# Optimization experiments

Measured on AMD Instinct MI355X. Metric: run time of the kernel, lower is better.

Reference implementation:

```python
import jax, jax.numpy as jnp
import numpy as np

HIDDEN = 2048
NUM_HEADS = 32
NUM_KV_HEADS = 8
GROUP = NUM_HEADS // NUM_KV_HEADS  # 4
HEAD_DIM = HIDDEN // NUM_HEADS     # 64
SEQ = 2048


def setup_inputs() -> dict:
    key = jax.random.key(0)
    ks = jax.random.split(key, 5)
    s = HIDDEN ** -0.5
    x = jax.random.normal(ks[0], (SEQ, HIDDEN), jnp.float32)
    q_proj = jax.random.normal(ks[1], (HIDDEN, HIDDEN), jnp.float32) * s
    k_proj = jax.random.normal(ks[2], (HIDDEN, HIDDEN // GROUP), jnp.float32) * s
    v_proj = jax.random.normal(ks[3], (HIDDEN, HIDDEN // GROUP), jnp.float32) * s
    o_proj = jax.random.normal(ks[4], (HIDDEN, HIDDEN), jnp.float32) * s
    # inv_freq = 1/rsqrt(10000**(i/d)) = sqrt(10000**(i/d)) per the original module
    inv_freq = jnp.sqrt(10000.0 ** (jnp.arange(0, HEAD_DIM, 2) / HEAD_DIM)).astype(jnp.float32)
    return {"x": x, "q_proj": q_proj, "k_proj": k_proj, "v_proj": v_proj,
            "o_proj": o_proj, "inv_freq": inv_freq}


def _rope(x, inv_freq):
    # x: [S, ..., HEAD_DIM]; rotation per the original (nonstandard) formula.
    orig_dtype = x.dtype
    x = x.astype(jnp.float32)
    seq = jnp.arange(x.shape[0])
    angles = seq[:, None] * jax.lax.stop_gradient(inv_freq)[None, :]  # [S, HEAD_DIM//2]
    bshape = (x.shape[0],) + (1,) * (x.ndim - 2) + (HEAD_DIM // 2,)
    sins = jnp.sin(angles).reshape(bshape)
    coss = jnp.cos(angles).reshape(bshape)
    half, odd = jnp.split(x, 2, axis=-1)
    out = jnp.concatenate([half * coss + odd * sins, half * sins - odd * coss], axis=-1)
    return out.astype(orig_dtype)


def reference(x, q_proj, k_proj, v_proj, o_proj, inv_freq):
    S = x.shape[0]
    q = (x @ q_proj).reshape(S, NUM_KV_HEADS, GROUP, HEAD_DIM)
    k = (x @ k_proj).reshape(S, NUM_KV_HEADS, HEAD_DIM)
    v = (x @ v_proj).reshape(S, NUM_KV_HEADS, HEAD_DIM)
    q = _rope(q, inv_freq)
    k = _rope(k, inv_freq)
    # scores: [a=S, b=S, h=kv_heads, g=group]
    scores = jnp.einsum('ahgd,bhd->abhg', q, k) / (HEAD_DIM ** 0.5)
    mask = jnp.tril(jnp.ones((S, S), dtype=jnp.bool_))[:, :, None, None]
    scores = jnp.where(mask, scores, -jnp.inf)
    attn = jax.nn.softmax(scores, axis=1)  # softmax over b (axis=-3)
    o = jnp.einsum('abhg,bhd->ahgd', attn, v).reshape(S, HIDDEN)
    return o @ o_proj
```

## Files before the change

kernel.cpp:

```cpp
#include <hip/hip_runtime.h>


typedef __bf16 bf16_t;
typedef __bf16 bf16x4 __attribute__((ext_vector_type(4)));
typedef __bf16 bf16x8 __attribute__((ext_vector_type(8)));
typedef float  f32x4  __attribute__((ext_vector_type(4)));
typedef short  s16x4  __attribute__((ext_vector_type(4)));

#define S_LEN   2048
#define HID     2048
#define NKV     8
#define NH      32
#define DHEAD   64
#define KVW     (NKV * DHEAD)

__device__ __align__(16) bf16_t g_xb [S_LEN * HID];
__device__ __align__(16) bf16_t g_wTq[HID * HID];
__device__ __align__(16) bf16_t g_wTk[KVW * HID];
__device__ __align__(16) bf16_t g_wTv[KVW * HID];
__device__ __align__(16) bf16_t g_wTo[HID * HID];
__device__ __align__(16) bf16_t g_q [S_LEN * HID];
__device__ __align__(16) bf16_t g_k [S_LEN * KVW];
__device__ __align__(16) bf16_t g_vT[KVW * S_LEN];
__device__ __align__(16) bf16_t g_om[S_LEN * HID];
__device__ float g_ropeC[S_LEN * 32];
__device__ float g_ropeS[S_LEN * 32];
__device__ __align__(16) float g_po[4u * S_LEN * HID];
__device__ float g_pl[4u * S_LEN * NH];

static __device__ inline s16x4 bc4(bf16x4 v) { s16x4 r; __builtin_memcpy(&r, &v, 8); return r; }

__device__ __forceinline__ void gll16(void* lds, const void* g) {
    __builtin_amdgcn_global_load_lds(
        (const __attribute__((address_space(1))) void*)g,
        (__attribute__((address_space(3))) void*)lds,
        16, 0, 0);
}

__global__ __launch_bounds__(256)
void prep_kernel(const float* __restrict__ x,
                 const float* __restrict__ qw, const float* __restrict__ kw,
                 const float* __restrict__ vw, const float* __restrict__ ow,
                 const void* __restrict__ invf_raw) {
    __shared__ bf16_t tile[64][65];
    int b = blockIdx.x, t = threadIdx.x;

    if (b < 256) {
        int idx = b * 256 + t;
        int s = idx >> 5, j = idx & 31;
        float f;
        if (*(const unsigned*)invf_raw == 0x3F800000u) {
            f = ((const float*)invf_raw)[j];
        } else {
            unsigned u = ((unsigned)((const unsigned short*)invf_raw)[j]) << 16;
            __builtin_memcpy(&f, &u, 4);
        }
        double a = (double)s * (double)f;
        g_ropeC[idx] = (float)cos(a);
        g_ropeS[idx] = (float)sin(a);
        return;
    }
    if (b < 4352) {
        int idx = (b - 256) * 256 + t;
        float4 v = reinterpret_cast<const float4*>(x)[idx];
        bf16x4 o;
        o[0] = (bf16_t)v.x; o[1] = (bf16_t)v.y; o[2] = (bf16_t)v.z; o[3] = (bf16_t)v.w;
        *reinterpret_cast<bf16x4*>(&g_xb[(size_t)idx * 4]) = o;
        return;
    }
    const float* in; bf16_t* outp; int R, C, tb;
    if (b < 5376)      { in = qw; outp = g_wTq; R = HID; C = HID; tb = b - 4352; }
    else if (b < 5632) { in = kw; outp = g_wTk; R = HID; C = KVW; tb = b - 5376; }
    else if (b < 5888) { in = vw; outp = g_wTv; R = HID; C = KVW; tb = b - 5632; }
    else               { in = ow; outp = g_wTo; R = HID; C = HID; tb = b - 5888; }
    int xt = C >> 6;
    int c0 = (tb % xt) * 64, r0 = (tb / xt) * 64;
    int tx = t & 63, ty = t >> 6;
    #pragma unroll
    for (int r = ty; r < 64; r += 4)
        tile[r][tx] = (bf16_t)in[(size_t)(r0 + r) * C + c0 + tx];
    __syncthreads();
    #pragma unroll
    for (int r = ty; r < 64; r += 4)
        outp[(size_t)(c0 + r) * R + r0 + tx] = tile[tx][r];
}

__global__ __launch_bounds__(256)
void gemm_fused_kernel(float* __restrict__ Cf, int which) {
    __shared__ __align__(16) bf16_t As[2][128 * 64];
    __shared__ __align__(16) bf16_t Bs[2][64 * 64];

    int t    = threadIdx.x;
    int lane = t & 63, wid = t >> 6;
    int quad = lane >> 4, l15 = lane & 15;

    int ntn  = (which == 1) ? 32 : 48;
    int nwg  = ntn * 16;
    int orig = blockIdx.x;
    int qq   = nwg >> 3;
    int wg   = (orig & 7) * qq + (orig >> 3);
    int my   = wg / ntn, nx = wg - my * ntn;
    int m0   = my * 128;

    const bf16_t* A; const bf16_t* Bt; int n0;
    if (which == 1)      { A = g_om; Bt = g_wTo; n0 = nx * 64; }
    else {
        A = g_xb;
        if (nx < 32)      { Bt = g_wTq; n0 = nx * 64; }
        else if (nx < 40) { Bt = g_wTk; n0 = (nx - 32) * 64; }
        else              { Bt = g_wTv; n0 = (nx - 40) * 64; }
    }

    int crow = lane >> 3;
    int gseg = (lane & 7) ^ crow;
    int so   = l15 & 7;
    int wm   = wid * 32;

    f32x4 acc[2][4];
    #pragma unroll
    for (int im = 0; im < 2; ++im)
        #pragma unroll
        for (int in = 0; in < 4; ++in)
            #pragma unroll
            for (int r = 0; r < 4; ++r) acc[im][in][r] = 0.f;

    auto stage = [&](int buf, int kt) {
        #pragma unroll
        for (int c = 0; c < 4; ++c)
            gll16(&As[buf][(wid * 4 + c) * 512],
                  A  + (size_t)(m0 + (wid * 4 + c) * 8 + crow) * HID + kt + gseg * 8);
        #pragma unroll
        for (int c = 0; c < 2; ++c)
            gll16(&Bs[buf][(wid * 2 + c) * 512],
                  Bt + (size_t)(n0 + (wid * 2 + c) * 8 + crow) * HID + kt + gseg * 8);
    };

    stage(0, 0);

    for (int it = 0; it < 32; ++it) {
        int cur = it & 1;
        if (it + 1 < 32) {
            stage(cur ^ 1, (it + 1) * 64);
            asm volatile("s_waitcnt vmcnt(6)" ::: "memory");
        } else {
            asm volatile("s_waitcnt vmcnt(0)" ::: "memory");
        }
        asm volatile("s_barrier" ::: "memory");

        #pragma unroll
        for (int kh = 0; kh < 2; ++kh) {
            bf16x8 af[2], bfv[4];
            #pragma unroll
            for (int i = 0; i < 2; ++i)
                af[i]  = *reinterpret_cast<const bf16x8*>(
                    &As[cur][(wm + i * 16 + l15) * 64 + (((kh * 4 + quad) ^ so) * 8)]);
            #pragma unroll
            for (int i = 0; i < 4; ++i)
                bfv[i] = *reinterpret_cast<const bf16x8*>(
                    &Bs[cur][(i * 16 + l15) * 64 + (((kh * 4 + quad) ^ so) * 8)]);
            #pragma unroll
            for (int im = 0; im < 2; ++im)
                #pragma unroll
                for (int in = 0; in < 4; ++in)
                    acc[im][in] = __builtin_amdgcn_mfma_f32_16x16x32_bf16(
                        af[im], bfv[in], acc[im][in], 0, 0, 0);
        }

        asm volatile("s_barrier" ::: "memory");
    }

    if (which == 1) {
        #pragma unroll
        for (int im = 0; im < 2; ++im) {
            int rowb = m0 + wm + im * 16 + quad * 4;
            #pragma unroll
            for (int in = 0; in < 4; ++in) {
                int col = n0 + in * 16 + l15;
                #pragma unroll
                for (int r = 0; r < 4; ++r)
                    Cf[(size_t)(rowb + r) * HID + col] = acc[im][in][r];
            }
        }
    } else if (nx < 40) {
        bf16_t* Cb; int N, colbase;
        if (nx < 32) { Cb = g_q; N = HID; colbase = nx * 64; }
        else         { Cb = g_k; N = KVW; colbase = (nx - 32) * 64; }
        #pragma unroll
        for (int im = 0; im < 2; ++im) {
            #pragma unroll
            for (int r = 0; r < 4; ++r) {
                int row = m0 + wm + im * 16 + quad * 4 + r;
                #pragma unroll
                for (int in = 0; in < 2; ++in) {
                    int d = in * 16 + l15;
                    float a  = acc[im][in][r];
                    float bb = acc[im][in + 2][r];
                    float cc = g_ropeC[row * 32 + d];
                    float ss = g_ropeS[row * 32 + d];
                    Cb[(size_t)row * N + colbase + d]      = (bf16_t)(a * cc + bb * ss);
                    Cb[(size_t)row * N + colbase + 32 + d] = (bf16_t)(a * ss - bb * cc);
                }
            }
        }
    } else {
        #pragma unroll
        for (int im = 0; im < 2; ++im) {
            int rowb = m0 + wm + im * 16 + quad * 4;
            #pragma unroll
            for (int in = 0; in < 4; ++in) {
                int col = (nx - 40) * 64 + in * 16 + l15;
                #pragma unroll
                for (int r = 0; r < 4; ++r)
                    g_vT[(size_t)col * S_LEN + (rowb + r)] = (bf16_t)acc[im][in][r];
            }
        }
    }
}

__global__ __launch_bounds__(256)
void flash_part_kernel() {
    __shared__ __align__(16) bf16_t Ks[2][64 * 64];
    __shared__ __align__(16) bf16_t Vs[2][64 * 64];

    int t    = threadIdx.x;
    int lane = t & 63, wid = t >> 6;
    int quad = lane >> 4, l15 = lane & 15;
    int bx   = blockIdx.x;
    int hk   = bx & 7;
    int qb32 = (bx >> 3) & 63;
    int chunk = bx >> 9;
    int nkt  = (qb32 >> 1) + 1;
    int kt0  = chunk * 8;
    if (kt0 >= nkt) return;
    int kt1  = min(kt0 + 8, nkt);
    int nt   = kt1 - kt0;

    int head = hk * 4 + wid;
    int q0   = qb32 * 32;

    int crow = lane >> 3;
    int gseg = (lane & 7) ^ crow;
    int so   = l15 & 7;

    bf16x8 aq[2][2];
    #pragma unroll
    for (int mq = 0; mq < 2; ++mq) {
        const bf16_t* qp = g_q + (size_t)(q0 + mq * 16 + l15) * HID + head * 64 + quad * 8;
        aq[mq][0] = *reinterpret_cast<const bf16x8*>(qp);
        aq[mq][1] = *reinterpret_cast<const bf16x8*>(qp + 32);
        #pragma unroll
        for (int j = 0; j < 8; ++j) {
            aq[mq][0][j] = (bf16_t)((float)aq[mq][0][j] * 0.125f);
            aq[mq][1][j] = (bf16_t)((float)aq[mq][1][j] * 0.125f);
        }
    }

    bf16x4 ones4;
    #pragma unroll
    for (int j = 0; j < 4; ++j) ones4[j] = (bf16_t)1.0f;
    s16x4 ones_s = bc4(ones4);

    f32x4 oacc[2][4], liacc[2];
    #pragma unroll
    for (int mq = 0; mq < 2; ++mq) {
        #pragma unroll
        for (int r = 0; r < 4; ++r) liacc[mq][r] = 0.f;
        #pragma unroll
        for (int dt = 0; dt < 4; ++dt)
            #pragma unroll
            for (int r = 0; r < 4; ++r) oacc[mq][dt][r] = 0.f;
    }

    int qcol[2] = { q0 + l15, q0 + 16 + l15 };

    auto stageKV = [&](int buf, int k0) {
        #pragma unroll
        for (int c = 0; c < 2; ++c) {
            int ch = wid * 2 + c;
            gll16(&Ks[buf][ch * 512],
                  g_k  + (size_t)(k0 + ch * 8 + crow) * KVW + hk * 64 + gseg * 8);
            gll16(&Vs[buf][ch * 512],
                  g_vT + (size_t)(hk * 64 + ch * 8 + crow) * S_LEN + k0 + gseg * 8);
        }
    };

    stageKV(0, kt0 * 64);

    for (int i = 0; i < nt; ++i) {
        int cur = i & 1;
        int k0  = (kt0 + i) * 64;
        if (i + 1 < nt) {
            stageKV(cur ^ 1, (kt0 + i + 1) * 64);
            asm volatile("s_waitcnt vmcnt(4)" ::: "memory");
        } else {
            asm volatile("s_waitcnt vmcnt(0)" ::: "memory");
        }
        asm volatile("s_barrier" ::: "memory");

        bf16x8 ak[4][2];
        #pragma unroll
        for (int mk = 0; mk < 4; ++mk) {
            int row = mk * 16 + l15;
            ak[mk][0] = *reinterpret_cast<const bf16x8*>(&Ks[cur][row * 64 + ((quad ^ so) * 8)]);
            ak[mk][1] = *reinterpret_cast<const bf16x8*>(&Ks[cur][row * 64 + (((4 + quad) ^ so) * 8)]);
        }

        f32x4 sacc[4][2];
        #pragma unroll
        for (int mk = 0; mk < 4; ++mk)
            #pragma unroll
            for (int mq = 0; mq < 2; ++mq) {
                f32x4 s;
                #pragma unroll
                for (int r = 0; r < 4; ++r) s[r] = 0.f;
                s = __builtin_amdgcn_mfma_f32_16x16x32_bf16(ak[mk][0], aq[mq][0], s, 0, 0, 0);
                s = __builtin_amdgcn_mfma_f32_16x16x32_bf16(ak[mk][1], aq[mq][1], s, 0, 0, 0);
                sacc[mk][mq] = s;
            }

        s16x4 pas[4][2];
        #pragma unroll
        for (int mk = 0; mk < 4; ++mk)
            #pragma unroll
            for (int mq = 0; mq < 2; ++mq) {
                bf16x4 pa;
                #pragma unroll
                for (int r = 0; r < 4; ++r) {
                    int kk = k0 + mk * 16 + quad * 4 + r;
                    pa[r] = (bf16_t)((kk <= qcol[mq]) ? __expf(sacc[mk][mq][r] - 16.0f) : 0.0f);
                }
                pas[mk][mq] = bc4(pa);
            }

        #pragma unroll
        for (int mk = 0; mk < 4; ++mk) {
            #pragma unroll
            for (int dt = 0; dt < 4; ++dt) {
                int rv = dt * 16 + l15;
                int vb = rv * 64 + (((mk * 2 + (quad >> 1)) ^ so) * 8) + (quad & 1) * 4;
                bf16x4 bv = *reinterpret_cast<const bf16x4*>(&Vs[cur][vb]);
                s16x4 bvs = bc4(bv);
                #pragma unroll
                for (int mq = 0; mq < 2; ++mq)
                    oacc[mq][dt] = __builtin_amdgcn_mfma_f32_16x16x16bf16_1k(pas[mk][mq], bvs, oacc[mq][dt], 0, 0, 0);
            }
            #pragma unroll
            for (int mq = 0; mq < 2; ++mq)
                liacc[mq] = __builtin_amdgcn_mfma_f32_16x16x16bf16_1k(pas[mk][mq], ones_s, liacc[mq], 0, 0, 0);
        }

        asm volatile("s_barrier" ::: "memory");
    }

    float* po = g_po + (size_t)chunk * S_LEN * HID;
    #pragma unroll
    for (int mq = 0; mq < 2; ++mq)
        #pragma unroll
        for (int r = 0; r < 4; ++r) {
            int row = q0 + mq * 16 + quad * 4 + r;
            #pragma unroll
            for (int dt = 0; dt < 4; ++dt)
                po[(size_t)row * HID + head * 64 + dt * 16 + l15] = oacc[mq][dt][r];
            if (l15 == 0)
                g_pl[((size_t)chunk * S_LEN + row) * NH + head] = liacc[mq][r];
        }
}

__global__ __launch_bounds__(256)
void flash_combine_kernel() {
    int t = blockIdx.x * 256 + threadIdx.x;
    int row  = t >> 9;
    int col4 = (t & 511) * 4;
    int head = col4 >> 6;
    int nkt  = ((row >> 5) >> 1) + 1;
    int nc   = (nkt + 7) >> 3;

    float4 s = make_float4(0.f, 0.f, 0.f, 0.f);
    float l = 0.f;
    for (int c = 0; c < nc; ++c) {
        const float4 v = *reinterpret_cast<const float4*>(
            g_po + ((size_t)c * S_LEN + row) * HID + col4);
        s.x += v.x; s.y += v.y; s.z += v.z; s.w += v.w;
        l += g_pl[((size_t)c * S_LEN + row) * NH + head];
    }
    float inv = 1.0f / l;
    bf16x4 o;
    o[0] = (bf16_t)(s.x * inv); o[1] = (bf16_t)(s.y * inv);
    o[2] = (bf16_t)(s.z * inv); o[3] = (bf16_t)(s.w * inv);
    *reinterpret_cast<bf16x4*>(&g_om[(size_t)row * HID + col4]) = o;
}

extern "C" void kernel_launch(void* const* d_in, const int* in_sizes, int n_in,
                              void* d_out, int out_size, void* d_ws, size_t ws_size,
                              hipStream_t stream) {
    const float* x    = (const float*)d_in[0];
    const float* qpW  = (const float*)d_in[1];
    const float* kpW  = (const float*)d_in[2];
    const float* vpW  = (const float*)d_in[3];
    const float* opW  = (const float*)d_in[4];
    const void*  invf = d_in[5];
    float* out = (float*)d_out;

    prep_kernel<<<6912, 256, 0, stream>>>(x, qpW, kpW, vpW, opW, invf);
    gemm_fused_kernel<<<768, 256, 0, stream>>>(nullptr, 0);
    flash_part_kernel<<<2048, 256, 0, stream>>>();
    flash_combine_kernel<<<4096, 256, 0, stream>>>();
    gemm_fused_kernel<<<512, 256, 0, stream>>>(out, 1);
}
```

Baseline: 246.4 us.

## Halve GEMM M-tile to 64x64 with 2x2 wave layout and MFMA priority hints

The GEMM kernel's output tile shrinks from 128x64 to 64x64, with waves arranged 2x2. The grid doubles for both the QKV projection and the output projection, which gives more workgroups and more parallelism on the GPU's many CUs. The price is less data reuse per tile, since each tile now runs 4 MFMAs per k-half instead of 8. s_setprio hints are also placed around the MFMA blocks in both the GEMM and the flash kernel. Separately, the RoPE angle is now computed in float before the double cos/sin, so it matches the reference's float32 angle rounding.

```diff
diff --git a/kernel.cpp b/kernel.cpp
--- a/kernel.cpp
+++ b/kernel.cpp
@@ -55,7 +55,8 @@
             unsigned u = ((unsigned)((const unsigned short*)invf_raw)[j]) << 16;
             __builtin_memcpy(&f, &u, 4);
         }
-        double a = (double)s * (double)f;
+        float a32 = (float)s * f;
+        double a = (double)a32;
         g_ropeC[idx] = (float)cos(a);
         g_ropeS[idx] = (float)sin(a);
         return;
@@ -87,7 +88,7 @@
 
 __global__ __launch_bounds__(256)
 void gemm_fused_kernel(float* __restrict__ Cf, int which) {
-    __shared__ __align__(16) bf16_t As[2][128 * 64];
+    __shared__ __align__(16) bf16_t As[2][64 * 64];
     __shared__ __align__(16) bf16_t Bs[2][64 * 64];
 
     int t    = threadIdx.x;
@@ -95,12 +96,12 @@
     int quad = lane >> 4, l15 = lane & 15;
 
     int ntn  = (which == 1) ? 32 : 48;
-    int nwg  = ntn * 16;
+    int nwg  = ntn * 32;
     int orig = blockIdx.x;
     int qq   = nwg >> 3;
     int wg   = (orig & 7) * qq + (orig >> 3);
     int my   = wg / ntn, nx = wg - my * ntn;
-    int m0   = my * 128;
+    int m0   = my * 64;
 
     const bf16_t* A; const bf16_t* Bt; int n0;
     if (which == 1)      { A = g_om; Bt = g_wTo; n0 = nx * 64; }
@@ -114,25 +115,26 @@
     int crow = lane >> 3;
     int gseg = (lane & 7) ^ crow;
     int so   = l15 & 7;
-    int wm   = wid * 32;
-
-    f32x4 acc[2][4];
+    int wr   = (wid >> 1) * 32;
+    int wc   = (wid & 1) * 16;
+
+    f32x4 acc[2][2];
     #pragma unroll
     for (int im = 0; im < 2; ++im)
         #pragma unroll
-        for (int in = 0; in < 4; ++in)
+        for (int in = 0; in < 2; ++in)
             #pragma unroll
             for (int r = 0; r < 4; ++r) acc[im][in][r] = 0.f;
 
     auto stage = [&](int buf, int kt) {
         #pragma unroll
-        for (int c = 0; c < 4; ++c)
-            gll16(&As[buf][(wid * 4 + c) * 512],
-                  A  + (size_t)(m0 + (wid * 4 + c) * 8 + crow) * HID + kt + gseg * 8);
-        #pragma unroll
-        for (int c = 0; c < 2; ++c)
-            gll16(&Bs[buf][(wid * 2 + c) * 512],
-                  Bt + (size_t)(n0 + (wid * 2 + c) * 8 + crow) * HID + kt + gseg * 8);
+        for (int c = 0; c < 2; ++c) {
+            int ch = wid * 2 + c;
+            gll16(&As[buf][ch * 512],
+                  A  + (size_t)(m0 + ch * 8 + crow) * HID + kt + gseg * 8);
+            gll16(&Bs[buf][ch * 512],
+                  Bt + (size_t)(n0 + ch * 8 + crow) * HID + kt + gseg * 8);
+        }
     };
 
     stage(0, 0);
@@ -141,7 +143,7 @@
         int cur = it & 1;
         if (it + 1 < 32) {
             stage(cur ^ 1, (it + 1) * 64);
-            asm volatile("s_waitcnt vmcnt(6)" ::: "memory");
+            asm volatile("s_waitcnt vmcnt(4)" ::: "memory");
         } else {
             asm volatile("s_waitcnt vmcnt(0)" ::: "memory");
         }
@@ -149,21 +151,23 @@
 
         #pragma unroll
         for (int kh = 0; kh < 2; ++kh) {
-            bf16x8 af[2], bfv[4];
-            #pragma unroll
-            for (int i = 0; i < 2; ++i)
-                af[i]  = *reinterpret_cast<const bf16x8*>(
-                    &As[cur][(wm + i * 16 + l15) * 64 + (((kh * 4 + quad) ^ so) * 8)]);
-            #pragma unroll
-            for (int i = 0; i < 4; ++i)
-                bfv[i] = *reinterpret_cast<const bf16x8*>(
-                    &Bs[cur][(i * 16 + l15) * 64 + (((kh * 4 + quad) ^ so) * 8)]);
+            bf16x8 af[2], bfv[2];
             #pragma unroll
             for (int im = 0; im < 2; ++im)
-                #pragma unroll
-                for (int in = 0; in < 4; ++in)
+                af[im]  = *reinterpret_cast<const bf16x8*>(
+                    &As[cur][(wr + im * 16 + l15) * 64 + (((kh * 4 + quad) ^ so) * 8)]);
+            #pragma unroll
+            for (int in = 0; in < 2; ++in)
+                bfv[in] = *reinterpret_cast<const bf16x8*>(
+                    &Bs[cur][(wc + in * 32 + l15) * 64 + (((kh * 4 + quad) ^ so) * 8)]);
+            __builtin_amdgcn_s_setprio(1);
+            #pragma unroll
+            for (int im = 0; im < 2; ++im)
+                #pragma unroll
+                for (int in = 0; in < 2; ++in)
                     acc[im][in] = __builtin_amdgcn_mfma_f32_16x16x32_bf16(
                         af[im], bfv[in], acc[im][in], 0, 0, 0);
+            __builtin_amdgcn_s_setprio(0);
         }
 
         asm volatile("s_barrier" ::: "memory");
@@ -172,10 +176,10 @@
     if (which == 1) {
         #pragma unroll
         for (int im = 0; im < 2; ++im) {
-            int rowb = m0 + wm + im * 16 + quad * 4;
-            #pragma unroll
-            for (int in = 0; in < 4; ++in) {
-                int col = n0 + in * 16 + l15;
+            int rowb = m0 + wr + im * 16 + quad * 4;
+            #pragma unroll
+            for (int in = 0; in < 2; ++in) {
+                int col = n0 + wc + in * 32 + l15;
                 #pragma unroll
                 for (int r = 0; r < 4; ++r)
                     Cf[(size_t)(rowb + r) * HID + col] = acc[im][in][r];
@@ -189,26 +193,23 @@
         for (int im = 0; im < 2; ++im) {
             #pragma unroll
             for (int r = 0; r < 4; ++r) {
-                int row = m0 + wm + im * 16 + quad * 4 + r;
-                #pragma unroll
-                for (int in = 0; in < 2; ++in) {
-                    int d = in * 16 + l15;
-                    float a  = acc[im][in][r];
-                    float bb = acc[im][in + 2][r];
-                    float cc = g_ropeC[row * 32 + d];
-                    float ss = g_ropeS[row * 32 + d];
-                    Cb[(size_t)row * N + colbase + d]      = (bf16_t)(a * cc + bb * ss);
-                    Cb[(size_t)row * N + colbase + 32 + d] = (bf16_t)(a * ss - bb * cc);
-                }
+                int row = m0 + wr + im * 16 + quad * 4 + r;
+                int d   = wc + l15;
+                float a  = acc[im][0][r];
+                float bb = acc[im][1][r];
+                float cc = g_ropeC[row * 32 + d];
+                float ss = g_ropeS[row * 32 + d];
+                Cb[(size_t)row * N + colbase + d]      = (bf16_t)(a * cc + bb * ss);
+                Cb[(size_t)row * N + colbase + 32 + d] = (bf16_t)(a * ss - bb * cc);
             }
         }
     } else {
         #pragma unroll
         for (int im = 0; im < 2; ++im) {
-            int rowb = m0 + wm + im * 16 + quad * 4;
-            #pragma unroll
-            for (int in = 0; in < 4; ++in) {
-                int col = (nx - 40) * 64 + in * 16 + l15;
+            int rowb = m0 + wr + im * 16 + quad * 4;
+            #pragma unroll
+            for (int in = 0; in < 2; ++in) {
+                int col = (nx - 40) * 64 + wc + in * 32 + l15;
                 #pragma unroll
                 for (int r = 0; r < 4; ++r)
                     g_vT[(size_t)col * S_LEN + (rowb + r)] = (bf16_t)acc[im][in][r];
@@ -306,6 +307,7 @@
         }
 
         f32x4 sacc[4][2];
+        __builtin_amdgcn_s_setprio(1);
         #pragma unroll
         for (int mk = 0; mk < 4; ++mk)
             #pragma unroll
@@ -317,6 +319,7 @@
                 s = __builtin_amdgcn_mfma_f32_16x16x32_bf16(ak[mk][1], aq[mq][1], s, 0, 0, 0);
                 sacc[mk][mq] = s;
             }
+        __builtin_amdgcn_s_setprio(0);
 
         s16x4 pas[4][2];
         #pragma unroll
@@ -332,6 +335,7 @@
                 pas[mk][mq] = bc4(pa);
             }
 
+        __builtin_amdgcn_s_setprio(1);
         #pragma unroll
         for (int mk = 0; mk < 4; ++mk) {
             #pragma unroll
@@ -348,6 +352,7 @@
             for (int mq = 0; mq < 2; ++mq)
                 liacc[mq] = __builtin_amdgcn_mfma_f32_16x16x16bf16_1k(pas[mk][mq], ones_s, liacc[mq], 0, 0, 0);
         }
+        __builtin_amdgcn_s_setprio(0);
 
         asm volatile("s_barrier" ::: "memory");
     }
@@ -402,8 +407,8 @@
     float* out = (float*)d_out;
 
     prep_kernel<<<6912, 256, 0, stream>>>(x, qpW, kpW, vpW, opW, invf);
-    gemm_fused_kernel<<<768, 256, 0, stream>>>(nullptr, 0);
+    gemm_fused_kernel<<<1536, 256, 0, stream>>>(nullptr, 0);
     flash_part_kernel<<<2048, 256, 0, stream>>>();
     flash_combine_kernel<<<4096, 256, 0, stream>>>();
-    gemm_fused_kernel<<<512, 256, 0, stream>>>(out, 1);
-}
+    gemm_fused_kernel<<<1024, 256, 0, stream>>>(out, 1);
+}
```

New measurement: 270.2 us. +9.7%, slower.

## Triple-buffer LDS in GEMM and flash kernels, vectorize weight transpose loads

Applied to the files above, without the earlier changes.

The GEMM and flash attention kernels move from two LDS buffers to three, prefetching two tiles ahead. Each loop now has one barrier instead of two, so loads overlap compute more and sync overhead drops. The prep transpose reads float4 vectors instead of scalars, and the RoPE angle is computed in float before the double trig. The cost is more LDS per block, which may lower occupancy, and the vmcnt counts must match the deeper pipeline.

```diff
diff --git a/kernel.cpp b/kernel.cpp
--- a/kernel.cpp
+++ b/kernel.cpp
@@ -55,7 +55,8 @@
             unsigned u = ((unsigned)((const unsigned short*)invf_raw)[j]) << 16;
             __builtin_memcpy(&f, &u, 4);
         }
-        double a = (double)s * (double)f;
+        float a32 = (float)s * f;
+        double a = (double)a32;
         g_ropeC[idx] = (float)cos(a);
         g_ropeS[idx] = (float)sin(a);
         return;
@@ -75,20 +76,27 @@
     else               { in = ow; outp = g_wTo; R = HID; C = HID; tb = b - 5888; }
     int xt = C >> 6;
     int c0 = (tb % xt) * 64, r0 = (tb / xt) * 64;
-    int tx = t & 63, ty = t >> 6;
-    #pragma unroll
-    for (int r = ty; r < 64; r += 4)
-        tile[r][tx] = (bf16_t)in[(size_t)(r0 + r) * C + c0 + tx];
+    int tx4 = t & 15, ty = t >> 4;
+    #pragma unroll
+    for (int r = ty; r < 64; r += 16) {
+        float4 v = *reinterpret_cast<const float4*>(
+            &in[(size_t)(r0 + r) * C + c0 + tx4 * 4]);
+        tile[r][tx4 * 4 + 0] = (bf16_t)v.x;
+        tile[r][tx4 * 4 + 1] = (bf16_t)v.y;
+        tile[r][tx4 * 4 + 2] = (bf16_t)v.z;
+        tile[r][tx4 * 4 + 3] = (bf16_t)v.w;
+    }
     __syncthreads();
-    #pragma unroll
-    for (int r = ty; r < 64; r += 4)
-        outp[(size_t)(c0 + r) * R + r0 + tx] = tile[tx][r];
+    int wx = t & 63, wy = t >> 6;
+    #pragma unroll
+    for (int r = wy; r < 64; r += 4)
+        outp[(size_t)(c0 + r) * R + r0 + wx] = tile[wx][r];
 }
 
 __global__ __launch_bounds__(256)
 void gemm_fused_kernel(float* __restrict__ Cf, int which) {
-    __shared__ __align__(16) bf16_t As[2][128 * 64];
-    __shared__ __align__(16) bf16_t Bs[2][64 * 64];
+    __shared__ __align__(16) bf16_t As[3][128 * 64];
+    __shared__ __align__(16) bf16_t Bs[3][64 * 64];
 
     int t    = threadIdx.x;
     int lane = t & 63, wid = t >> 6;
@@ -136,16 +144,15 @@
     };
 
     stage(0, 0);
+    stage(1, 64);
 
     for (int it = 0; it < 32; ++it) {
-        int cur = it & 1;
-        if (it + 1 < 32) {
-            stage(cur ^ 1, (it + 1) * 64);
-            asm volatile("s_waitcnt vmcnt(6)" ::: "memory");
-        } else {
-            asm volatile("s_waitcnt vmcnt(0)" ::: "memory");
-        }
+        int cur = it % 3;
+        if (it + 1 < 32) { asm volatile("s_waitcnt vmcnt(6)" ::: "memory"); }
+        else             { asm volatile("s_waitcnt vmcnt(0)" ::: "memory"); }
         asm volatile("s_barrier" ::: "memory");
+        if (it + 2 < 32)
+            stage((it + 2) % 3, (it + 2) * 64);
 
         #pragma unroll
         for (int kh = 0; kh < 2; ++kh) {
@@ -165,8 +172,6 @@
                     acc[im][in] = __builtin_amdgcn_mfma_f32_16x16x32_bf16(
                         af[im], bfv[in], acc[im][in], 0, 0, 0);
         }
-
-        asm volatile("s_barrier" ::: "memory");
     }
 
     if (which == 1) {
@@ -219,8 +224,8 @@
 
 __global__ __launch_bounds__(256)
 void flash_part_kernel() {
-    __shared__ __align__(16) bf16_t Ks[2][64 * 64];
-    __shared__ __align__(16) bf16_t Vs[2][64 * 64];
+    __shared__ __align__(16) bf16_t Ks[3][64 * 64];
+    __shared__ __align__(16) bf16_t Vs[3][64 * 64];
 
     int t    = threadIdx.x;
     int lane = t & 63, wid = t >> 6;
@@ -285,17 +290,16 @@
     };
 
     stageKV(0, kt0 * 64);
+    if (nt > 1) stageKV(1, (kt0 + 1) * 64);
 
     for (int i = 0; i < nt; ++i) {
-        int cur = i & 1;
+        int cur = i % 3;
         int k0  = (kt0 + i) * 64;
-        if (i + 1 < nt) {
-            stageKV(cur ^ 1, (kt0 + i + 1) * 64);
-            asm volatile("s_waitcnt vmcnt(4)" ::: "memory");
-        } else {
-            asm volatile("s_waitcnt vmcnt(0)" ::: "memory");
-        }
+        if (i + 1 < nt) { asm volatile("s_waitcnt vmcnt(4)" ::: "memory"); }
+        else            { asm volatile("s_waitcnt vmcnt(0)" ::: "memory"); }
         asm volatile("s_barrier" ::: "memory");
+        if (i + 2 < nt)
+            stageKV((i + 2) % 3, (kt0 + i + 2) * 64);
 
         bf16x8 ak[4][2];
         #pragma unroll
@@ -348,8 +352,6 @@
             for (int mq = 0; mq < 2; ++mq)
                 liacc[mq] = __builtin_amdgcn_mfma_f32_16x16x16bf16_1k(pas[mk][mq], ones_s, liacc[mq], 0, 0, 0);
         }
-
-        asm volatile("s_barrier" ::: "memory");
     }
 
     float* po = g_po + (size_t)chunk * S_LEN * HID;
```

New measurement: 268.8 us. 1.09x slower.

## Split flash KV range across two wave groups in-block, drop global combine kernel

Applied to the files above, without the earlier changes.

Rewrites the attention kernel to use 512-thread blocks in which two 4-wave groups handle alternating KV tiles for the same 32 query rows. The two partial results are merged through shared memory instead of through global fp32 partial buffers and a separate combine kernel. Query blocks are ordered so long and short causal rows are interleaved for load balance. It also vectorises the fp32 loads in the weight transpose and computes the rope angle in fp32. The cost is twice the LDS per block, fewer blocks in flight, and the full causal range for a row now runs inside a single block.

```diff
diff --git a/kernel.cpp b/kernel.cpp
--- a/kernel.cpp
+++ b/kernel.cpp
@@ -25,8 +25,6 @@
 __device__ __align__(16) bf16_t g_om[S_LEN * HID];
 __device__ float g_ropeC[S_LEN * 32];
 __device__ float g_ropeS[S_LEN * 32];
-__device__ __align__(16) float g_po[4u * S_LEN * HID];
-__device__ float g_pl[4u * S_LEN * NH];
 
 static __device__ inline s16x4 bc4(bf16x4 v) { s16x4 r; __builtin_memcpy(&r, &v, 8); return r; }
 
@@ -55,7 +53,8 @@
             unsigned u = ((unsigned)((const unsigned short*)invf_raw)[j]) << 16;
             __builtin_memcpy(&f, &u, 4);
         }
-        double a = (double)s * (double)f;
+        float a32 = (float)s * f;
+        double a = (double)a32;
         g_ropeC[idx] = (float)cos(a);
         g_ropeS[idx] = (float)sin(a);
         return;
@@ -75,14 +74,21 @@
     else               { in = ow; outp = g_wTo; R = HID; C = HID; tb = b - 5888; }
     int xt = C >> 6;
     int c0 = (tb % xt) * 64, r0 = (tb / xt) * 64;
-    int tx = t & 63, ty = t >> 6;
-    #pragma unroll
-    for (int r = ty; r < 64; r += 4)
-        tile[r][tx] = (bf16_t)in[(size_t)(r0 + r) * C + c0 + tx];
+    int tx4 = t & 15, ty = t >> 4;
+    #pragma unroll
+    for (int r = ty; r < 64; r += 16) {
+        float4 v = *reinterpret_cast<const float4*>(
+            &in[(size_t)(r0 + r) * C + c0 + tx4 * 4]);
+        tile[r][tx4 * 4 + 0] = (bf16_t)v.x;
+        tile[r][tx4 * 4 + 1] = (bf16_t)v.y;
+        tile[r][tx4 * 4 + 2] = (bf16_t)v.z;
+        tile[r][tx4 * 4 + 3] = (bf16_t)v.w;
+    }
     __syncthreads();
-    #pragma unroll
-    for (int r = ty; r < 64; r += 4)
-        outp[(size_t)(c0 + r) * R + r0 + tx] = tile[tx][r];
+    int wx = t & 63, wy = t >> 6;
+    #pragma unroll
+    for (int r = wy; r < 64; r += 4)
+        outp[(size_t)(c0 + r) * R + r0 + wx] = tile[wx][r];
 }
 
 __global__ __launch_bounds__(256)
@@ -217,25 +223,23 @@
     }
 }
 
-__global__ __launch_bounds__(256)
+__global__ __launch_bounds__(512)
 void flash_part_kernel() {
-    __shared__ __align__(16) bf16_t Ks[2][64 * 64];
-    __shared__ __align__(16) bf16_t Vs[2][64 * 64];
+    __shared__ __align__(16) bf16_t SM[2][2][2][64 * 64];
 
     int t    = threadIdx.x;
     int lane = t & 63, wid = t >> 6;
+    int g    = wid >> 2;
+    int wh   = wid & 3;
     int quad = lane >> 4, l15 = lane & 15;
     int bx   = blockIdx.x;
     int hk   = bx & 7;
-    int qb32 = (bx >> 3) & 63;
-    int chunk = bx >> 9;
+    int slot = bx >> 3;
+    int qb32 = (slot & 1) ? (slot >> 1) : (63 - (slot >> 1));
     int nkt  = (qb32 >> 1) + 1;
-    int kt0  = chunk * 8;
-    if (kt0 >= nkt) return;
-    int kt1  = min(kt0 + 8, nkt);
-    int nt   = kt1 - kt0;
-
-    int head = hk * 4 + wid;
+    int ng   = (nkt + 1) >> 1;
+
+    int head = hk * 4 + wh;
     int q0   = qb32 * 32;
 
     int crow = lane >> 3;
@@ -276,118 +280,119 @@
     auto stageKV = [&](int buf, int k0) {
         #pragma unroll
         for (int c = 0; c < 2; ++c) {
-            int ch = wid * 2 + c;
-            gll16(&Ks[buf][ch * 512],
+            int ch = wh * 2 + c;
+            gll16(&SM[g][0][buf][ch * 512],
                   g_k  + (size_t)(k0 + ch * 8 + crow) * KVW + hk * 64 + gseg * 8);
-            gll16(&Vs[buf][ch * 512],
+            gll16(&SM[g][1][buf][ch * 512],
                   g_vT + (size_t)(hk * 64 + ch * 8 + crow) * S_LEN + k0 + gseg * 8);
         }
     };
 
-    stageKV(0, kt0 * 64);
-
-    for (int i = 0; i < nt; ++i) {
-        int cur = i & 1;
-        int k0  = (kt0 + i) * 64;
-        if (i + 1 < nt) {
-            stageKV(cur ^ 1, (kt0 + i + 1) * 64);
+    if (g < nkt) stageKV(0, g * 64);
+
+    for (int i = 0; i < ng; ++i) {
+        int cur  = i & 1;
+        int kt   = 2 * i + g;
+        bool live = (kt < nkt);
+        int ktn  = kt + 2;
+        bool stage_next = (i + 1 < ng) && (ktn < nkt);
+        if (stage_next) {
+            stageKV(cur ^ 1, ktn * 64);
             asm volatile("s_waitcnt vmcnt(4)" ::: "memory");
         } else {
             asm volatile("s_waitcnt vmcnt(0)" ::: "memory");
         }
         asm volatile("s_barrier" ::: "memory");
 
-        bf16x8 ak[4][2];
-        #pragma unroll
-        for (int mk = 0; mk < 4; ++mk) {
-            int row = mk * 16 + l15;
-            ak[mk][0] = *reinterpret_cast<const bf16x8*>(&Ks[cur][row * 64 + ((quad ^ so) * 8)]);
-            ak[mk][1] = *reinterpret_cast<const bf16x8*>(&Ks[cur][row * 64 + (((4 + quad) ^ so) * 8)]);
-        }
-
-        f32x4 sacc[4][2];
-        #pragma unroll
-        for (int mk = 0; mk < 4; ++mk)
-            #pragma unroll
-            for (int mq = 0; mq < 2; ++mq) {
-                f32x4 s;
-                #pragma unroll
-                for (int r = 0; r < 4; ++r) s[r] = 0.f;
-                s = __builtin_amdgcn_mfma_f32_16x16x32_bf16(ak[mk][0], aq[mq][0], s, 0, 0, 0);
-                s = __builtin_amdgcn_mfma_f32_16x16x32_bf16(ak[mk][1], aq[mq][1], s, 0, 0, 0);
-                sacc[mk][mq] = s;
-            }
-
-        s16x4 pas[4][2];
-        #pragma unroll
-        for (int mk = 0; mk < 4; ++mk)
-            #pragma unroll
-            for (int mq = 0; mq < 2; ++mq) {
-                bf16x4 pa;
-                #pragma unroll
-                for (int r = 0; r < 4; ++r) {
-                    int kk = k0 + mk * 16 + quad * 4 + r;
-                    pa[r] = (bf16_t)((kk <= qcol[mq]) ? __expf(sacc[mk][mq][r] - 16.0f) : 0.0f);
+        if (live) {
+            int k0 = kt * 64;
+            bf16x8 ak[4][2];
+            #pragma unroll
+            for (int mk = 0; mk < 4; ++mk) {
+                int row = mk * 16 + l15;
+                ak[mk][0] = *reinterpret_cast<const bf16x8*>(&SM[g][0][cur][row * 64 + ((quad ^ so) * 8)]);
+                ak[mk][1] = *reinterpret_cast<const bf16x8*>(&SM[g][0][cur][row * 64 + (((4 + quad) ^ so) * 8)]);
+            }
+
+            f32x4 sacc[4][2];
+            #pragma unroll
+            for (int mk = 0; mk < 4; ++mk)
+                #pragma unroll
+                for (int mq = 0; mq < 2; ++mq) {
+                    f32x4 s;
+                    #pragma unroll
+                    for (int r = 0; r < 4; ++r) s[r] = 0.f;
+                    s = __builtin_amdgcn_mfma_f32_16x16x32_bf16(ak[mk][0], aq[mq][0], s, 0, 0, 0);
+                    s = __builtin_amdgcn_mfma_f32_16x16x32_bf16(ak[mk][1], aq[mq][1], s, 0, 0, 0);
+                    sacc[mk][mq] = s;
                 }
-                pas[mk][mq] = bc4(pa);
-            }
-
-        #pragma unroll
-        for (int mk = 0; mk < 4; ++mk) {
-            #pragma unroll
-            for (int dt = 0; dt < 4; ++dt) {
-                int rv = dt * 16 + l15;
-                int vb = rv * 64 + (((mk * 2 + (quad >> 1)) ^ so) * 8) + (quad & 1) * 4;
-                bf16x4 bv = *reinterpret_cast<const bf16x4*>(&Vs[cur][vb]);
-                s16x4 bvs = bc4(bv);
+
+            s16x4 pas[4][2];
+            #pragma unroll
+            for (int mk = 0; mk < 4; ++mk)
+                #pragma unroll
+                for (int mq = 0; mq < 2; ++mq) {
+                    bf16x4 pa;
+                    #pragma unroll
+                    for (int r = 0; r < 4; ++r) {
+                        int kk = k0 + mk * 16 + quad * 4 + r;
+                        pa[r] = (bf16_t)((kk <= qcol[mq]) ? __expf(sacc[mk][mq][r] - 16.0f) : 0.0f);
+                    }
+                    pas[mk][mq] = bc4(pa);
+                }
+
+            #pragma unroll
+            for (int mk = 0; mk < 4; ++mk) {
+                #pragma unroll
+                for (int dt = 0; dt < 4; ++dt) {
+                    int rv = dt * 16 + l15;
+                    int vb = rv * 64 + (((mk * 2 + (quad >> 1)) ^ so) * 8) + (quad & 1) * 4;
+                    bf16x4 bv = *reinterpret_cast<const bf16x4*>(&SM[g][1][cur][vb]);
+                    s16x4 bvs = bc4(bv);
+                    #pragma unroll
+                    for (int mq = 0; mq < 2; ++mq)
+                        oacc[mq][dt] = __builtin_amdgcn_mfma_f32_16x16x16bf16_1k(pas[mk][mq], bvs, oacc[mq][dt], 0, 0, 0);
+                }
                 #pragma unroll
                 for (int mq = 0; mq < 2; ++mq)
-                    oacc[mq][dt] = __builtin_amdgcn_mfma_f32_16x16x16bf16_1k(pas[mk][mq], bvs, oacc[mq][dt], 0, 0, 0);
-            }
-            #pragma unroll
-            for (int mq = 0; mq < 2; ++mq)
-                liacc[mq] = __builtin_amdgcn_mfma_f32_16x16x16bf16_1k(pas[mk][mq], ones_s, liacc[mq], 0, 0, 0);
+                    liacc[mq] = __builtin_amdgcn_mfma_f32_16x16x16bf16_1k(pas[mk][mq], ones_s, liacc[mq], 0, 0, 0);
+            }
         }
 
         asm volatile("s_barrier" ::: "memory");
     }
 
-    float* po = g_po + (size_t)chunk * S_LEN * HID;
-    #pragma unroll
-    for (int mq = 0; mq < 2; ++mq)
-        #pragma unroll
-        for (int r = 0; r < 4; ++r) {
-            int row = q0 + mq * 16 + quad * 4 + r;
-            #pragma unroll
-            for (int dt = 0; dt < 4; ++dt)
-                po[(size_t)row * HID + head * 64 + dt * 16 + l15] = oacc[mq][dt][r];
-            if (l15 == 0)
-                g_pl[((size_t)chunk * S_LEN + row) * NH + head] = liacc[mq][r];
-        }
-}
-
-__global__ __launch_bounds__(256)
-void flash_combine_kernel() {
-    int t = blockIdx.x * 256 + threadIdx.x;
-    int row  = t >> 9;
-    int col4 = (t & 511) * 4;
-    int head = col4 >> 6;
-    int nkt  = ((row >> 5) >> 1) + 1;
-    int nc   = (nkt + 7) >> 3;
-
-    float4 s = make_float4(0.f, 0.f, 0.f, 0.f);
-    float l = 0.f;
-    for (int c = 0; c < nc; ++c) {
-        const float4 v = *reinterpret_cast<const float4*>(
-            g_po + ((size_t)c * S_LEN + row) * HID + col4);
-        s.x += v.x; s.y += v.y; s.z += v.z; s.w += v.w;
-        l += g_pl[((size_t)c * S_LEN + row) * NH + head];
-    }
-    float inv = 1.0f / l;
-    bf16x4 o;
-    o[0] = (bf16_t)(s.x * inv); o[1] = (bf16_t)(s.y * inv);
-    o[2] = (bf16_t)(s.z * inv); o[3] = (bf16_t)(s.w * inv);
-    *reinterpret_cast<bf16x4*>(&g_om[(size_t)row * HID + col4]) = o;
+    float* pO = reinterpret_cast<float*>(&SM[1][0][0][0]);
+    float* pl = reinterpret_cast<float*>(&SM[0][0][0][0]);
+    if (g == 1) {
+        #pragma unroll
+        for (int mq = 0; mq < 2; ++mq)
+            #pragma unroll
+            for (int r = 0; r < 4; ++r) {
+                int row = mq * 16 + quad * 4 + r;
+                #pragma unroll
+                for (int dt = 0; dt < 4; ++dt)
+                    pO[(wh * 32 + row) * 64 + dt * 16 + l15] = oacc[mq][dt][r];
+                if (l15 == 0) pl[wh * 32 + row] = liacc[mq][r];
+            }
+    }
+    asm volatile("s_waitcnt lgkmcnt(0)" ::: "memory");
+    asm volatile("s_barrier" ::: "memory");
+    if (g == 0) {
+        #pragma unroll
+        for (int mq = 0; mq < 2; ++mq)
+            #pragma unroll
+            for (int r = 0; r < 4; ++r) {
+                int row = mq * 16 + quad * 4 + r;
+                float l = liacc[mq][r] + pl[wh * 32 + row];
+                float inv = 1.0f / l;
+                #pragma unroll
+                for (int dt = 0; dt < 4; ++dt) {
+                    float o = oacc[mq][dt][r] + pO[(wh * 32 + row) * 64 + dt * 16 + l15];
+                    g_om[(size_t)(q0 + row) * HID + head * 64 + dt * 16 + l15] = (bf16_t)(o * inv);
+                }
+            }
+    }
 }
 
 extern "C" void kernel_launch(void* const* d_in, const int* in_sizes, int n_in,
@@ -403,7 +408,6 @@
 
     prep_kernel<<<6912, 256, 0, stream>>>(x, qpW, kpW, vpW, opW, invf);
     gemm_fused_kernel<<<768, 256, 0, stream>>>(nullptr, 0);
-    flash_part_kernel<<<2048, 256, 0, stream>>>();
-    flash_combine_kernel<<<4096, 256, 0, stream>>>();
+    flash_part_kernel<<<512, 512, 0, stream>>>();
     gemm_fused_kernel<<<512, 256, 0, stream>>>(out, 1);
 }
```

After: 245.2 us. No clear change (-0.5%).
